# Optimization experiments

Measured on AMD Instinct MI355X. Metric: run time of the kernel, lower is better.

## Reference

```python
import jax, jax.numpy as jnp
import numpy as np

B, T, C = 2, 2048, 1024
H = 16
D = C // H  # head_dim = 64


def setup_inputs() -> dict:
    key = jax.random.key(0)
    k1, k2, k3, k4, k5 = jax.random.split(key, 5)
    s = 0.02
    return {
        "x": jax.random.normal(k1, (B, T, C), dtype=jnp.float32),
        "w_qkv": jax.random.normal(k2, (C, 3 * C), dtype=jnp.float32) * s,
        "b_qkv": jnp.zeros((3 * C,), dtype=jnp.float32),
        "w_proj": jax.random.normal(k3, (C, C), dtype=jnp.float32) * s,
        "b_proj": jnp.zeros((C,), dtype=jnp.float32),
    }


def reference(x, w_qkv, b_qkv, w_proj, b_proj):
    b, t, c = x.shape
    qkv = x @ w_qkv + b_qkv                      # [B,T,3C]
    q, k, v = jnp.split(qkv, 3, axis=-1)
    # [B,T,C] -> [B,H,T,D]
    q = q.reshape(b, t, H, D).transpose(0, 2, 1, 3)
    k = k.reshape(b, t, H, D).transpose(0, 2, 1, 3)
    v = v.reshape(b, t, H, D).transpose(0, 2, 1, 3)
    att = jnp.einsum("bhqd,bhkd->bhqk", q, k) / jnp.sqrt(jnp.float32(D))
    causal = jnp.tril(jnp.ones((t, t), dtype=bool))  # True where allowed
    att = jnp.where(causal, att, -jnp.inf)
    att = jax.nn.softmax(att, axis=-1)
    out = jnp.einsum("bhqk,bhkd->bhqd", att, v)      # [B,H,T,D]
    out = out.transpose(0, 2, 1, 3).reshape(b, t, c)
    return out @ w_proj + b_proj
```

## Files before the change

kernel.cpp:

```cpp
#include <hip/hip_runtime.h>
#include <hip/hip_bf16.h>
#include <math.h>
#include <stdint.h>

#define B_ 2
#define T_ 2048
#define C_ 1024
#define H_ 16
#define D_ 64

typedef __attribute__((ext_vector_type(8))) short bf16x8;
typedef __attribute__((ext_vector_type(4))) float f32x4;

__device__ inline short f2bf(float f) {
  __hip_bfloat16 h = __float2bfloat16(f);
  return *(short*)&h;
}

__device__ inline void async16(const void* g, void* l) {
  __builtin_amdgcn_global_load_lds(
      (const __attribute__((address_space(1))) uint32_t*)g,
      (__attribute__((address_space(3))) uint32_t*)l, 16, 0, 0);
}


__global__ __launch_bounds__(256) void prep(
    const float* __restrict__ X, const float* __restrict__ Wq,
    const float* __restrict__ Wp, short* __restrict__ Xb,
    short* __restrict__ Wqt, short* __restrict__ Wpt) {
  const int tid = threadIdx.x;
  const int blk = blockIdx.x;
  __shared__ short Ts[64][68];

  if (blk < 512) {
    const int g = tid >> 3;
    const int sub = tid & 7;
    const int sc = sub >> 1;
    const int e4 = (sub & 1) * 4;
#pragma unroll
    for (int pass = 0; pass < 8; ++pass) {
      const int m = blk * 8 + pass;
      float4 v = *(const float4*)(X + (size_t)m * C_ + tid * 4);
      const int xv = (m >> 1) & 3;
      short o[4] = {f2bf(v.x), f2bf(v.y), f2bf(v.z), f2bf(v.w)};
      *(uint2*)(Xb + (size_t)m * C_ + g * 32 + ((sc ^ xv) << 3) + e4) =
          *(uint2*)o;
    }
    return;
  }

  const float* W;
  short* Wt;
  int N, n0, k0;
  if (blk < 1280) {
    int i = blk - 512;
    W = Wq; Wt = Wqt; N = 3 * C_;
    n0 = (i % 48) * 64; k0 = (i / 48) * 64;
  } else {
    int i = blk - 1280;
    W = Wp; Wt = Wpt; N = C_;
    n0 = (i & 15) * 64; k0 = (i >> 4) * 64;
  }
  {
    int r = tid >> 2, c0 = (tid & 3) * 16;
    const float* src = W + (size_t)(k0 + r) * N + n0 + c0;
#pragma unroll
    for (int u = 0; u < 16; u += 4) {
      float4 v = *(const float4*)(src + u);
      Ts[r][c0 + u + 0] = f2bf(v.x);
      Ts[r][c0 + u + 1] = f2bf(v.y);
      Ts[r][c0 + u + 2] = f2bf(v.z);
      Ts[r][c0 + u + 3] = f2bf(v.w);
    }
  }
  __syncthreads();
#pragma unroll
  for (int p = 0; p < 2; ++p) {
    int n = (tid >> 3) + p * 32;
    int kc = tid & 7;
    int xv = ((n0 + n) >> 1) & 3;
    int ka = kc * 8;
    int dk = (ka & ~31) | ((((ka >> 3) & 3) ^ xv) << 3);
    short tmp[8];
#pragma unroll
    for (int u = 0; u < 8; ++u) tmp[u] = Ts[ka + u][n];
    *(uint4*)(Wt + (size_t)(n0 + n) * 1024 + k0 + dk) = *(uint4*)tmp;
  }
}

template <int N, int BN, bool QKV>
__global__ __launch_bounds__(256) void gemm_mfma(
    const short* __restrict__ A, const short* __restrict__ Bt,
    const float* __restrict__ bias, short* __restrict__ Qp,
    short* __restrict__ Kp, short* __restrict__ Vp, float* __restrict__ Cout) {
  constexpr int NJ = BN / 32;
  constexpr int BI = BN * 32;
  const int tid = threadIdx.x;
  const int wave = tid >> 6, lane = tid & 63;
  const int quad = lane >> 4, l16 = lane & 15;
  const int wm = wave >> 1, wn = wave & 1;
  const int m0 = blockIdx.y * 128, n0 = blockIdx.x * BN;

  __shared__ short As[2][4096];
  __shared__ short Bs[2][BI];

  const int srow = tid >> 2, skc = tid & 3;
  const size_t arow0 = (size_t)(m0 + srow) * 1024 + skc * 8;
  const size_t brow0 = (size_t)(n0 + srow) * 1024 + skc * 8;

  f32x4 acc[4][NJ] = {};

  const int xi = quad ^ ((l16 >> 1) & 3);
  int aoff[4], boff[NJ];
#pragma unroll
  for (int i = 0; i < 4; ++i) aoff[i] = (wm * 64 + i * 16 + l16) * 32 + xi * 8;
#pragma unroll
  for (int j = 0; j < NJ; ++j)
    boff[j] = (wn * (BN / 2) + j * 16 + l16) * 32 + xi * 8;

  for (int k0 = 0; k0 < 1024; k0 += 64) {
    __syncthreads();
#pragma unroll
    for (int f = 0; f < 2; ++f) {
      const int kf = k0 + f * 32;
      async16(A + arow0 + kf, &As[f][tid * 8]);
      async16(A + arow0 + (size_t)64 * 1024 + kf, &As[f][2048 + tid * 8]);
      async16(Bt + brow0 + kf, &Bs[f][tid * 8]);
      if (BN == 128)
        async16(Bt + brow0 + (size_t)64 * 1024 + kf, &Bs[f][2048 + tid * 8]);
    }
    __syncthreads();

#pragma unroll
    for (int f = 0; f < 2; ++f) {
      bf16x8 af[4], bfr[NJ];
#pragma unroll
      for (int i = 0; i < 4; ++i) af[i] = *(const bf16x8*)&As[f][aoff[i]];
#pragma unroll
      for (int j = 0; j < NJ; ++j) bfr[j] = *(const bf16x8*)&Bs[f][boff[j]];
#pragma unroll
      for (int i = 0; i < 4; ++i)
#pragma unroll
        for (int j = 0; j < NJ; ++j)
          acc[i][j] = __builtin_amdgcn_mfma_f32_16x16x32_bf16(
              af[i], bfr[j], acc[i][j], 0, 0, 0);
    }
  }

  float bj[NJ];
#pragma unroll
  for (int j = 0; j < NJ; ++j) bj[j] = bias[n0 + wn * (BN / 2) + j * 16 + l16];

  if (QKV) {
#pragma unroll
    for (int i = 0; i < 4; ++i) {
#pragma unroll
      for (int reg = 0; reg < 4; ++reg) {
        int m = m0 + wm * 64 + i * 16 + quad * 4 + reg;
        int b = m >> 11, t = m & (T_ - 1);
#pragma unroll
        for (int j = 0; j < NJ; ++j) {
          int n = n0 + wn * (BN / 2) + j * 16 + l16;
          float v = acc[i][j][reg] + bj[j];
          int sel = n >> 10, cc = n & (C_ - 1);
          int hh = cc >> 6, d = cc & 63;
          size_t base = (size_t)(b * H_ + hh) * 131072 + (size_t)(t >> 6) * 4096;
          if (sel == 0) {
            Qp[base + (d >> 3) * 512 + (t & 63) * 8 + (d & 7)] =
                f2bf(v * 0.18033688011112042f);
          } else if (sel == 1) {
            Kp[base + (d >> 3) * 512 + (t & 63) * 8 + (d & 7)] = f2bf(v);
          } else {
            Vp[base + ((t & 63) >> 3) * 512 + d * 8 + (t & 7)] = f2bf(v);
          }
        }
      }
    }
  } else {
#pragma unroll
    for (int i = 0; i < 4; ++i) {
#pragma unroll
      for (int reg = 0; reg < 4; ++reg) {
        int m = m0 + wm * 64 + i * 16 + quad * 4 + reg;
#pragma unroll
        for (int j = 0; j < NJ; ++j) {
          int n = n0 + wn * (BN / 2) + j * 16 + l16;
          Cout[(size_t)m * N + n] = acc[i][j][reg] + bj[j];
        }
      }
    }
  }
}

__global__ __launch_bounds__(256, 2) void attn_kernel(
    const short* __restrict__ Qt, const short* __restrict__ Kt,
    const short* __restrict__ Vt, short* __restrict__ attb) {
  const int tid = threadIdx.x;
  const int wave = tid >> 6, lane = tid & 63;
  const int quad = lane >> 4, l16 = lane & 15;

  const int blk = blockIdx.x;
  const int bh = blk & 31;
  const int i = blk >> 5;
  const int pj = (i < 8) ? (15 - i) : (i - 8);
  const int NT = 2 * pj + 2;
  const int h = bh & 15, b = bh >> 4;

  const short* Qg = Qt + (size_t)bh * 131072;
  const short* Kg = Kt + (size_t)bh * 131072;
  const short* Vg = Vt + (size_t)bh * 131072;

  __shared__ short Ks[2][4096];
  __shared__ short Vs[2][4096];
  __shared__ short Ps[2][4096];

  const int rowl = 16 * wave + l16;

  bf16x8 bq[2][2];
#pragma unroll
  for (int g = 0; g < 2; ++g)
#pragma unroll
    for (int f = 0; f < 2; ++f)
      bq[g][f] = *(const bf16x8*)(Qg +
                 (size_t)((2 * pj + g) * 8 + 4 * f + quad) * 512 + rowl * 8);

  async16(Kg + tid * 8, &Ks[0][tid * 8]);
  async16(Kg + 2048 + tid * 8, &Ks[0][2048 + tid * 8]);
  async16(Vg + tid * 8, &Vs[0][tid * 8]);
  async16(Vg + 2048 + tid * 8, &Vs[0][2048 + tid * 8]);

  f32x4 oacc[4][2] = {};
  float lsum[2] = {0.f, 0.f};

  auto stage_next = [&](int kt) {
    const int dst = (kt + 1) & 1;
    const short* kp = Kg + (size_t)(kt + 1) * 4096;
    const short* vp = Vg + (size_t)(kt + 1) * 4096;
    async16(kp + tid * 8, &Ks[dst][tid * 8]);
    async16(kp + 2048 + tid * 8, &Ks[dst][2048 + tid * 8]);
    async16(vp + tid * 8, &Vs[dst][tid * 8]);
    async16(vp + 2048 + tid * 8, &Vs[dst][2048 + tid * 8]);
  };

  auto qkt2 = [&](int buf, f32x4 (&sacc)[4][2]) {
    __builtin_amdgcn_s_setprio(1);
#pragma unroll
    for (int c = 0; c < 4; ++c) {
#pragma unroll
      for (int f = 0; f < 2; ++f) {
        bf16x8 ak =
            *(const bf16x8*)&Ks[buf][((4 * f + quad) * 64 + 16 * c + l16) * 8];
        sacc[c][0] = __builtin_amdgcn_mfma_f32_16x16x32_bf16(
            ak, bq[0][f], sacc[c][0], 0, 0, 0);
        sacc[c][1] = __builtin_amdgcn_mfma_f32_16x16x32_bf16(
            ak, bq[1][f], sacc[c][1], 0, 0, 0);
      }
    }
    __builtin_amdgcn_s_setprio(0);
  };

  auto smax = [&](f32x4 (&sacc)[4][2], int g, bool mask) {
#pragma unroll
    for (int c = 0; c < 4; ++c) {
      short4 pk;
#pragma unroll
      for (int reg = 0; reg < 4; ++reg) {
        int keyl = 16 * c + 4 * quad + reg;
        float p = (mask && keyl > rowl)
                      ? 0.f
                      : __builtin_amdgcn_exp2f(sacc[c][g][reg]);
        lsum[g] += p;
        ((short*)&pk)[reg] = f2bf(p);
      }
      *(short4*)&Ps[g][(2 * c + (quad >> 1)) * 512 + rowl * 8 + (quad & 1) * 4] =
          pk;
    }
  };

  auto pv2 = [&](int buf) {
    __asm__ volatile("s_waitcnt lgkmcnt(0)" ::: "memory");
    bf16x8 ap[2][2];
#pragma unroll
    for (int f = 0; f < 2; ++f) {
      ap[0][f] = *(const bf16x8*)&Ps[0][(4 * f + quad) * 512 + rowl * 8];
      ap[1][f] = *(const bf16x8*)&Ps[1][(4 * f + quad) * 512 + rowl * 8];
    }
    __builtin_amdgcn_s_setprio(1);
#pragma unroll
    for (int n = 0; n < 4; ++n) {
#pragma unroll
      for (int f = 0; f < 2; ++f) {
        bf16x8 bv =
            *(const bf16x8*)&Vs[buf][((4 * f + quad) * 64 + 16 * n + l16) * 8];
        oacc[n][0] = __builtin_amdgcn_mfma_f32_16x16x32_bf16(
            ap[0][f], bv, oacc[n][0], 0, 0, 0);
        oacc[n][1] = __builtin_amdgcn_mfma_f32_16x16x32_bf16(
            ap[1][f], bv, oacc[n][1], 0, 0, 0);
      }
    }
    __builtin_amdgcn_s_setprio(0);
  };

  for (int kt = 0; kt < NT - 2; ++kt) {
    const int buf = kt & 1;
    __syncthreads();
    stage_next(kt);
    f32x4 sacc[4][2] = {};
    qkt2(buf, sacc);
    smax(sacc, 0, false);
    smax(sacc, 1, false);
    pv2(buf);
  }
  {
    const int kt = NT - 2, buf = kt & 1;
    __syncthreads();
    stage_next(kt);
    f32x4 sacc[4][2] = {};
    qkt2(buf, sacc);
    smax(sacc, 0, true);
    smax(sacc, 1, false);
    pv2(buf);
  }
  {
    const int buf = (NT - 1) & 1;
    __syncthreads();
    f32x4 sacc1[4] = {};
    __builtin_amdgcn_s_setprio(1);
#pragma unroll
    for (int c = 0; c < 4; ++c)
#pragma unroll
      for (int f = 0; f < 2; ++f) {
        bf16x8 ak =
            *(const bf16x8*)&Ks[buf][((4 * f + quad) * 64 + 16 * c + l16) * 8];
        sacc1[c] = __builtin_amdgcn_mfma_f32_16x16x32_bf16(
            ak, bq[1][f], sacc1[c], 0, 0, 0);
      }
    __builtin_amdgcn_s_setprio(0);
#pragma unroll
    for (int c = 0; c < 4; ++c) {
      short4 pk;
#pragma unroll
      for (int reg = 0; reg < 4; ++reg) {
        int keyl = 16 * c + 4 * quad + reg;
        float p = (keyl > rowl) ? 0.f : __builtin_amdgcn_exp2f(sacc1[c][reg]);
        lsum[1] += p;
        ((short*)&pk)[reg] = f2bf(p);
      }
      *(short4*)&Ps[1][(2 * c + (quad >> 1)) * 512 + rowl * 8 + (quad & 1) * 4] =
          pk;
    }
    __asm__ volatile("s_waitcnt lgkmcnt(0)" ::: "memory");
    bf16x8 ap1[2];
#pragma unroll
    for (int f = 0; f < 2; ++f)
      ap1[f] = *(const bf16x8*)&Ps[1][(4 * f + quad) * 512 + rowl * 8];
    __builtin_amdgcn_s_setprio(1);
#pragma unroll
    for (int n = 0; n < 4; ++n)
#pragma unroll
      for (int f = 0; f < 2; ++f) {
        bf16x8 bv =
            *(const bf16x8*)&Vs[buf][((4 * f + quad) * 64 + 16 * n + l16) * 8];
        oacc[n][1] = __builtin_amdgcn_mfma_f32_16x16x32_bf16(
            ap1[f], bv, oacc[n][1], 0, 0, 0);
      }
    __builtin_amdgcn_s_setprio(0);
  }

#pragma unroll
  for (int g = 0; g < 2; ++g) {
    float ls = lsum[g];
    ls += __shfl_xor(ls, 16);
    ls += __shfl_xor(ls, 32);
    float linv[4];
#pragma unroll
    for (int reg = 0; reg < 4; ++reg)
      linv[reg] = 1.0f / __shfl(ls, 4 * quad + reg, 64);
#pragma unroll
    for (int reg = 0; reg < 4; ++reg) {
      const int row = (2 * pj + g) * 64 + 16 * wave + 4 * quad + reg;
      const int m = b * T_ + row;
      const int xv = (m >> 1) & 3;
#pragma unroll
      for (int n = 0; n < 4; ++n) {
        int c = h * 64 + 16 * n + l16;
        int cs = (c & ~31) | ((((c >> 3) & 3) ^ xv) << 3) | (c & 7);
        attb[(size_t)m * C_ + cs] = f2bf(oacc[n][g][reg] * linv[reg]);
      }
    }
  }
}

extern "C" void kernel_launch(void* const* d_in, const int* in_sizes, int n_in,
                              void* d_out, int out_size, void* d_ws, size_t ws_size,
                              hipStream_t stream) {
  const float* x      = (const float*)d_in[0];
  const float* w_qkv  = (const float*)d_in[1];
  const float* b_qkv  = (const float*)d_in[2];
  const float* w_proj = (const float*)d_in[3];
  const float* b_proj = (const float*)d_in[4];
  float* out = (float*)d_out;

  const size_t per = (size_t)B_ * H_ * T_ * D_;
  short* Qp   = (short*)d_ws;
  short* Kp   = Qp + per;
  short* Vp   = Kp + per;
  short* attb = Vp + per;
  short* xb   = attb + per;
  short* wqt  = xb + per;
  short* wpt  = wqt + (size_t)3 * C_ * C_;

  prep<<<1536, 256, 0, stream>>>(x, w_qkv, w_proj, xb, wqt, wpt);

  gemm_mfma<3 * C_, 128, true><<<dim3(24, 32), 256, 0, stream>>>(
      xb, wqt, b_qkv, Qp, Kp, Vp, nullptr);

  attn_kernel<<<dim3(512), 256, 0, stream>>>(Qp, Kp, Vp, attb);

  gemm_mfma<C_, 64, false><<<dim3(16, 32), 256, 0, stream>>>(
      attb, wpt, b_proj, nullptr, nullptr, nullptr, out);
}
```

Measured before the change: 179.4 us.

## Pipeline GEMM k-loop with triple-buffered async LDS loads

Replaces the GEMM's load-then-compute loop with a three-stage ring buffer. The next 32-wide k-slice is issued through global_load_lds while the current one is computed, using explicit vmcnt waits and a single barrier per step. This targets the exposed global-load latency and the double barrier per iteration. It also raises the launch-bounds occupancy hint to 3 blocks and uses more LDS. Correctness relies on the hand-written vmcnt counts and on the three-buffer reuse distance avoiding overwrites of a stage still being read.

```diff
diff --git a/kernel.cpp b/kernel.cpp
--- a/kernel.cpp
+++ b/kernel.cpp
@@ -89,7 +89,7 @@
 }
 
 template <int N, int BN, bool QKV>
-__global__ __launch_bounds__(256) void gemm_mfma(
+__global__ __launch_bounds__(256, 3) void gemm_mfma(
     const short* __restrict__ A, const short* __restrict__ Bt,
     const float* __restrict__ bias, short* __restrict__ Qp,
     short* __restrict__ Kp, short* __restrict__ Vp, float* __restrict__ Cout) {
@@ -101,8 +101,8 @@
   const int wm = wave >> 1, wn = wave & 1;
   const int m0 = blockIdx.y * 128, n0 = blockIdx.x * BN;
 
-  __shared__ short As[2][4096];
-  __shared__ short Bs[2][BI];
+  __shared__ short As[3][4096];
+  __shared__ short Bs[3][BI];
 
   const int srow = tid >> 2, skc = tid & 3;
   const size_t arow0 = (size_t)(m0 + srow) * 1024 + skc * 8;
@@ -118,33 +118,41 @@
   for (int j = 0; j < NJ; ++j)
     boff[j] = (wn * (BN / 2) + j * 16 + l16) * 32 + xi * 8;
 
-  for (int k0 = 0; k0 < 1024; k0 += 64) {
-    __syncthreads();
-#pragma unroll
-    for (int f = 0; f < 2; ++f) {
-      const int kf = k0 + f * 32;
-      async16(A + arow0 + kf, &As[f][tid * 8]);
-      async16(A + arow0 + (size_t)64 * 1024 + kf, &As[f][2048 + tid * 8]);
-      async16(Bt + brow0 + kf, &Bs[f][tid * 8]);
-      if (BN == 128)
-        async16(Bt + brow0 + (size_t)64 * 1024 + kf, &Bs[f][2048 + tid * 8]);
-    }
-    __syncthreads();
-
-#pragma unroll
-    for (int f = 0; f < 2; ++f) {
-      bf16x8 af[4], bfr[NJ];
-#pragma unroll
-      for (int i = 0; i < 4; ++i) af[i] = *(const bf16x8*)&As[f][aoff[i]];
-#pragma unroll
-      for (int j = 0; j < NJ; ++j) bfr[j] = *(const bf16x8*)&Bs[f][boff[j]];
-#pragma unroll
-      for (int i = 0; i < 4; ++i)
-#pragma unroll
-        for (int j = 0; j < NJ; ++j)
-          acc[i][j] = __builtin_amdgcn_mfma_f32_16x16x32_bf16(
-              af[i], bfr[j], acc[i][j], 0, 0, 0);
-    }
+  auto stage = [&](int t) {
+    const int s = t % 3;
+    const size_t kf = (size_t)t * 32;
+    async16(A + arow0 + kf, &As[s][tid * 8]);
+    async16(A + arow0 + (size_t)64 * 1024 + kf, &As[s][2048 + tid * 8]);
+    async16(Bt + brow0 + kf, &Bs[s][tid * 8]);
+    if (BN == 128)
+      async16(Bt + brow0 + (size_t)64 * 1024 + kf, &Bs[s][2048 + tid * 8]);
+  };
+
+  stage(0);
+  for (int t = 0; t < 32; ++t) {
+    const int s = t % 3;
+    if (t + 1 < 32) {
+      stage(t + 1);
+      if constexpr (BN == 128)
+        __asm__ volatile("s_waitcnt vmcnt(4)" ::: "memory");
+      else
+        __asm__ volatile("s_waitcnt vmcnt(3)" ::: "memory");
+    } else {
+      __asm__ volatile("s_waitcnt vmcnt(0)" ::: "memory");
+    }
+    __builtin_amdgcn_s_barrier();
+
+    bf16x8 af[4], bfr[NJ];
+#pragma unroll
+    for (int i = 0; i < 4; ++i) af[i] = *(const bf16x8*)&As[s][aoff[i]];
+#pragma unroll
+    for (int j = 0; j < NJ; ++j) bfr[j] = *(const bf16x8*)&Bs[s][boff[j]];
+#pragma unroll
+    for (int i = 0; i < 4; ++i)
+#pragma unroll
+      for (int j = 0; j < NJ; ++j)
+        acc[i][j] = __builtin_amdgcn_mfma_f32_16x16x32_bf16(
+            af[i], bfr[j], acc[i][j], 0, 0, 0);
   }
 
   float bj[NJ];
```

New measurement: 179.1 us. Within noise of the previous version (-0.2%).
